# Optimization experiments

Measured on AMD Instinct MI355X. Metric: run time of the kernel, lower is better.

## Reference

```python
import jax, jax.numpy as jnp
import numpy as np

NBITS = 4
QN, QP = -(2 ** (NBITS - 1)), 2 ** (NBITS - 1) - 1  # -8, 7
NUM_HEADS = 12


def round_ste(x):
    # round_pass: straight-through estimator round
    return x + jax.lax.stop_gradient(jnp.round(x) - x)


def act3b(x, alpha, bias=0.0, signed=True):
    qn, qp = (-4.0, 3.0) if signed else (0.0, 7.0)
    return round_ste(jnp.clip((x + bias) / alpha, qn, qp))


def setup_inputs() -> dict:
    key = jax.random.key(0)
    ks = jax.random.split(key, 20)
    B, N, C, H = 32, 512, 768, NUM_HEADS
    hd = C // H
    u = lambda k, s: jax.random.uniform(k, s, jnp.float32, 0.05, 0.15)
    return {
        'x0': jax.random.normal(ks[0], (B, N, C), jnp.float32),
        'qkv_w': 0.02 * jax.random.normal(ks[1], (3 * C, C), jnp.float32),
        'qkv_alpha': u(ks[2], (3 * C,)),
        'qkv_bias': 0.02 * jax.random.normal(ks[3], (3 * C,), jnp.float32),
        'qkv_act_alpha': u(ks[4], (C,)),
        'proj_w': 0.02 * jax.random.normal(ks[5], (C, C), jnp.float32),
        'proj_alpha': u(ks[6], (C,)),
        'proj_bias': 0.02 * jax.random.normal(ks[7], (C,), jnp.float32),
        'proj_act_alpha': u(ks[8], (C,)),
        'normq_w': jax.random.uniform(ks[9], (hd,), jnp.float32, 0.8, 1.2),
        'normq_b': 0.01 * jax.random.normal(ks[10], (hd,), jnp.float32),
        'normk_w': jax.random.uniform(ks[11], (hd,), jnp.float32, 0.8, 1.2),
        'normk_b': 0.01 * jax.random.normal(ks[12], (hd,), jnp.float32),
        'qact_alpha': u(ks[13], (H,)),
        'kact_alpha': u(ks[14], (H,)),
        'vact_alpha': u(ks[15], (H,)),
        'attnact_alpha': u(ks[16], (H,)),
    }


def reference(x0, qkv_w, qkv_alpha, qkv_bias, qkv_act_alpha, proj_w, proj_alpha,
              proj_bias, proj_act_alpha, normq_w, normq_b, normk_w, normk_b,
              qact_alpha, kact_alpha, vact_alpha, attnact_alpha):
    B, N, C = x0.shape
    H = NUM_HEADS
    hd = C // H
    scale = hd ** -0.5

    # input activation quant (ActQ_v2, nbits=4)
    a_in = qkv_act_alpha.mean()
    x0_q = round_ste(jnp.clip(x0 / a_in, QN, QP))
    # kernel-wise 4-bit weight quant for qkv (no dequant here; scales folded later)
    w_q = round_ste(jnp.clip(qkv_w / qkv_alpha[:, None], QN, QP))
    qkv = x0_q @ w_q.T
    # integer-domain bias (truncated toward zero, like .int())
    qkv = qkv + jnp.trunc(qkv_bias / a_in / qkv_alpha)

    qkv = qkv.reshape(B, N, 3, H, hd).transpose(2, 0, 3, 1, 4)  # [3,B,H,N,hd]
    q0, k0, v0 = qkv[0], qkv[1], qkv[2]
    alpha3 = qkv_alpha.reshape(3, H, 1, hd)

    # fused scaled LayerNorm + 3-bit quant for q and k
    def norm_quant(x, ch_scale, nw, nb, act_a):
        xs = x * ch_scale  # [B,H,N,hd]
        centered = xs - xs.mean(-1, keepdims=True)
        std = jnp.std(xs, axis=-1, ddof=1, keepdims=True)
        return act3b(centered / (std + 1e-5), alpha=act_a / nw, bias=nb / nw)

    q2 = norm_quant(q0, alpha3[0], normq_w, normq_b, qact_alpha.mean())
    k2 = norm_quant(k0, alpha3[1], normk_w, normk_b, kact_alpha.mean())
    v2 = act3b(v0, alpha=vact_alpha.mean() / (a_in * alpha3[2]))

    # integer QK^T
    qk = jnp.einsum('bhqd,bhkd->bhqk', q2, k2)

    # base-2 softmax approximation
    div = 128.0
    sm_scale = scale * qact_alpha.mean() * kact_alpha.mean()
    e = jnp.trunc((1.0 / np.log(2)) * sm_scale * qk * div)
    attn_exp = jnp.exp2(jnp.round(e / div))
    attn = act3b(attn_exp / attn_exp.sum(-1, keepdims=True),
                 alpha=attnact_alpha.mean(), signed=False)

    # integer AV
    x1 = jnp.einsum('bhqk,bhkd->bhqd', attn, v2)
    x1 = x1.transpose(0, 2, 1, 3).reshape(B, N, C)
    x1_q = act3b(x1, alpha=proj_act_alpha.mean() / (attnact_alpha.mean() * vact_alpha.mean()))

    pw_q = round_ste(jnp.clip(proj_w / proj_alpha[:, None], QN, QP))
    out = (x1_q @ pw_q.T) * proj_alpha * proj_act_alpha.mean() + proj_bias
    return out
```

## Files before the change

### kernel.cpp

```cpp
#include <hip/hip_runtime.h>
#include <stdint.h>


#define BB 32
#define NN 512
#define CC 768
#define HH 12
#define HD 64
#define M_ROWS (BB * NN)
#define QKV_C (3 * CC)
#define KTA ((size_t)M_ROWS * 64)
#define KTB ((size_t)QKV_C * 64)
#define KTP ((size_t)CC * 64)

typedef int v4i __attribute__((ext_vector_type(4)));
typedef int v16i __attribute__((ext_vector_type(16)));

__device__ __forceinline__ float fadd(float a, float b) { return __fadd_rn(a, b); }
__device__ __forceinline__ float fmul(float a, float b) { return __fmul_rn(a, b); }
__device__ __forceinline__ float fdiv(float a, float b) { return __fdiv_rn(a, b); }
__device__ __forceinline__ float fsub(float a, float b) { return __fsub_rn(a, b); }

__device__ float np_sum_96(const float* a) {
  float r[8];
#pragma unroll
  for (int j = 0; j < 8; j++) r[j] = a[j];
  for (int i = 8; i < 96; i += 8)
#pragma unroll
    for (int j = 0; j < 8; j++) r[j] = fadd(r[j], a[i + j]);
  return fadd(fadd(fadd(r[0], r[1]), fadd(r[2], r[3])),
              fadd(fadd(r[4], r[5]), fadd(r[6], r[7])));
}

__device__ float np_mean_12(const float* a) {
  float r[8];
#pragma unroll
  for (int j = 0; j < 8; j++) r[j] = a[j];
  float res = fadd(fadd(fadd(r[0], r[1]), fadd(r[2], r[3])),
                   fadd(fadd(r[4], r[5]), fadd(r[6], r[7])));
  res = fadd(res, a[8]);
  res = fadd(res, a[9]);
  res = fadd(res, a[10]);
  res = fadd(res, a[11]);
  return fdiv(res, 12.0f);
}

__global__ void prep_kernel(const float* __restrict__ qkv_act_alpha,
                            const float* __restrict__ proj_act_alpha,
                            const float* __restrict__ qact_alpha,
                            const float* __restrict__ kact_alpha,
                            const float* __restrict__ vact_alpha,
                            const float* __restrict__ attnact_alpha,
                            const float* __restrict__ normq_w,
                            const float* __restrict__ normq_b,
                            const float* __restrict__ normk_w,
                            const float* __restrict__ normk_b,
                            const float* __restrict__ qkv_bias,
                            const float* __restrict__ qkv_alpha,
                            float* __restrict__ scal,
                            float* __restrict__ qparams,
                            float* __restrict__ biasq) {
  __shared__ float s_scal[8];
  __shared__ float chunk[16];
  int tid = threadIdx.x;
  if (tid < 8) chunk[tid] = np_sum_96(qkv_act_alpha + 96 * tid);
  else if (tid < 16) chunk[tid] = np_sum_96(proj_act_alpha + 96 * (tid - 8));
  if (tid == 16) s_scal[1] = np_mean_12(qact_alpha);
  if (tid == 17) s_scal[2] = np_mean_12(kact_alpha);
  if (tid == 18) s_scal[3] = np_mean_12(vact_alpha);
  if (tid == 19) s_scal[4] = np_mean_12(attnact_alpha);
  __syncthreads();
  if (tid == 0) {
    float s0 = fadd(fadd(chunk[0], chunk[1]), fadd(chunk[2], chunk[3]));
    float s1 = fadd(fadd(chunk[4], chunk[5]), fadd(chunk[6], chunk[7]));
    s_scal[0] = fdiv(fadd(s0, s1), 768.0f);
    float p0 = fadd(fadd(chunk[8], chunk[9]), fadd(chunk[10], chunk[11]));
    float p1 = fadd(fadd(chunk[12], chunk[13]), fadd(chunk[14], chunk[15]));
    s_scal[5] = fdiv(fadd(p0, p1), 768.0f);
  }
  __syncthreads();
  if (tid < 6) scal[tid] = s_scal[tid];
  if (tid < 64) {
    qparams[tid]       = fdiv(s_scal[1], normq_w[tid]);
    qparams[64 + tid]  = fdiv(normq_b[tid], normq_w[tid]);
    qparams[128 + tid] = fdiv(s_scal[2], normk_w[tid]);
    qparams[192 + tid] = fdiv(normk_b[tid], normk_w[tid]);
  }
  float a_in = s_scal[0];
  for (int c = tid; c < QKV_C; c += blockDim.x)
    biasq[c] = truncf(fdiv(fdiv(qkv_bias[c], a_in), qkv_alpha[c]));
}

__device__ __forceinline__ size_t fragaddr(int row, int b) {
  return (size_t)(row & ~31) * 64 + ((b >> 4) * 512 + (row & 31) * 16 + (b & 15));
}

__global__ void quant_x0_kernel(const float* __restrict__ x0,
                                const float* __restrict__ scal,
                                int8_t* __restrict__ x0q, int total4) {
  int i = blockIdx.x * blockDim.x + threadIdx.x;
  if (i >= total4) return;
  float a_in = scal[0];
  float4 v = ((const float4*)x0)[i];
  char4 o;
  o.x = (int8_t)rintf(fminf(fmaxf(fdiv(v.x, a_in), -8.f), 7.f));
  o.y = (int8_t)rintf(fminf(fmaxf(fdiv(v.y, a_in), -8.f), 7.f));
  o.z = (int8_t)rintf(fminf(fmaxf(fdiv(v.z, a_in), -8.f), 7.f));
  o.w = (int8_t)rintf(fminf(fmaxf(fdiv(v.w, a_in), -8.f), 7.f));
  int seq = i / 192;
  int kp = (i - seq * 192) * 4;
  int b = kp & 63;
  *(char4*)(x0q + (size_t)(kp >> 6) * KTA + fragaddr(seq, b)) = o;
}

__global__ void quant_w_kernel(const float* __restrict__ w,
                               const float* __restrict__ alpha,
                               int8_t* __restrict__ wq, int rows, int total) {
  int i = blockIdx.x * blockDim.x + threadIdx.x;
  if (i >= total) return;
  int row = i / CC;
  int k = i - row * CC;
  float t = fminf(fmaxf(fdiv(w[i], alpha[row]), -8.f), 7.f);
  wq[(size_t)(k >> 6) * ((size_t)rows * 64) + fragaddr(row, k)] =
      (int8_t)rintf(t);
}

__global__ __launch_bounds__(256, 5) void gemm_qkv_kernel(
    const int8_t* __restrict__ Aq, const int8_t* __restrict__ Wq,
    const float* __restrict__ biasq, const float* __restrict__ scal,
    const float* __restrict__ qkv_alpha, const float* __restrict__ qparams,
    int8_t* __restrict__ q2, int8_t* __restrict__ k2,
    int8_t* __restrict__ v2t) {
  __shared__ __align__(16) int8_t packT[4][3072];

  const int L = blockIdx.x;
  const int xcd = L & 7, s = L >> 3;
  const int rb = xcd + 8 * (s / 36);
  const int g = s % 36;
  const int tid = threadIdx.x;
  const int w = tid >> 6, lane = tid & 63;
  const int l31 = lane & 31, hi = lane >> 5;
  const int sec = g / HH, head = g % HH;
  const int col0 = g * 64;
  const int b_idx = rb >> 2, nbase = (rb & 3) * 128;
  const int w32 = w * 32;
  const size_t bh = (size_t)b_idx * HH + head;

  v16i acc0 = (v16i)(0), acc1 = (v16i)(0);

  const int8_t* pa = Aq + (size_t)(rb * 128 + w32) * 64 + hi * 512 + l31 * 16;
  const int8_t* pb = Wq + (size_t)col0 * 64 + hi * 512 + l31 * 16;

  if (sec < 2) {
    v4i Aa = *(const v4i*)(pa);
    v4i Ab = *(const v4i*)(pa + 1024);
    v4i B0a = *(const v4i*)(pb);
    v4i B0b = *(const v4i*)(pb + 1024);
    v4i B1a = *(const v4i*)(pb + 2048);
    v4i B1b = *(const v4i*)(pb + 3072);
#pragma unroll 1
    for (int kt = 0; kt < 11; kt++) {
      const int8_t* npa = pa + (size_t)(kt + 1) * KTA;
      const int8_t* npb = pb + (size_t)(kt + 1) * KTB;
      v4i nAa = *(const v4i*)(npa);
      v4i nAb = *(const v4i*)(npa + 1024);
      v4i nB0a = *(const v4i*)(npb);
      v4i nB0b = *(const v4i*)(npb + 1024);
      v4i nB1a = *(const v4i*)(npb + 2048);
      v4i nB1b = *(const v4i*)(npb + 3072);
      acc0 = __builtin_amdgcn_mfma_i32_32x32x32_i8(B0a, Aa, acc0, 0, 0, 0);
      acc1 = __builtin_amdgcn_mfma_i32_32x32x32_i8(B1a, Aa, acc1, 0, 0, 0);
      acc0 = __builtin_amdgcn_mfma_i32_32x32x32_i8(B0b, Ab, acc0, 0, 0, 0);
      acc1 = __builtin_amdgcn_mfma_i32_32x32x32_i8(B1b, Ab, acc1, 0, 0, 0);
      Aa = nAa; Ab = nAb; B0a = nB0a; B0b = nB0b; B1a = nB1a; B1b = nB1b;
    }
    acc0 = __builtin_amdgcn_mfma_i32_32x32x32_i8(B0a, Aa, acc0, 0, 0, 0);
    acc1 = __builtin_amdgcn_mfma_i32_32x32x32_i8(B1a, Aa, acc1, 0, 0, 0);
    acc0 = __builtin_amdgcn_mfma_i32_32x32x32_i8(B0b, Ab, acc0, 0, 0, 0);
    acc1 = __builtin_amdgcn_mfma_i32_32x32x32_i8(B1b, Ab, acc1, 0, 0, 0);
    float xs[2][16];
#pragma unroll
    for (int i = 0; i < 2; i++)
#pragma unroll
      for (int b = 0; b < 4; b++) {
        int cg = col0 + 32 * i + 8 * b + 4 * hi;
        float4 bqv = *(const float4*)(biasq + cg);
        float4 alv = *(const float4*)(qkv_alpha + cg);
        const float* bqp = (const float*)&bqv;
        const float* alp = (const float*)&alv;
#pragma unroll
        for (int c = 0; c < 4; c++) {
          int av = (i == 0) ? acc0[4 * b + c] : acc1[4 * b + c];
          xs[i][4 * b + c] = fmul(fadd((float)av, bqp[c]), alp[c]);
        }
      }
    float rc[4];
#pragma unroll
    for (int c = 0; c < 4; c++) rc[c] = xs[0][c];
#pragma unroll
    for (int b = 1; b < 4; b++)
#pragma unroll
      for (int c = 0; c < 4; c++) rc[c] = fadd(rc[c], xs[0][4 * b + c]);
#pragma unroll
    for (int b = 0; b < 4; b++)
#pragma unroll
      for (int c = 0; c < 4; c++) rc[c] = fadd(rc[c], xs[1][4 * b + c]);
    float Ls = fadd(fadd(rc[0], rc[1]), fadd(rc[2], rc[3]));
    float Rs = __shfl_xor(Ls, 32, 64);
    float mn = fdiv(fadd(Ls, Rs), 64.0f);
    float vc[4];
#pragma unroll
    for (int c = 0; c < 4; c++) {
      float d = fsub(xs[0][c], mn);
      vc[c] = fmul(d, d);
    }
#pragma unroll
    for (int b = 1; b < 4; b++)
#pragma unroll
      for (int c = 0; c < 4; c++) {
        float d = fsub(xs[0][4 * b + c], mn);
        vc[c] = fadd(vc[c], fmul(d, d));
      }
#pragma unroll
    for (int b = 0; b < 4; b++)
#pragma unroll
      for (int c = 0; c < 4; c++) {
        float d = fsub(xs[1][4 * b + c], mn);
        vc[c] = fadd(vc[c], fmul(d, d));
      }
    float Lv = fadd(fadd(vc[0], vc[1]), fadd(vc[2], vc[3]));
    float Rv = __shfl_xor(Lv, 32, 64);
    float var = fdiv(fadd(Lv, Rv), 63.0f);
    float den = fadd(__fsqrt_rn(var), 1e-5f);
    const float* ap = qparams + (sec == 0 ? 0 : 128);
#pragma unroll
    for (int i = 0; i < 2; i++)
#pragma unroll
      for (int b = 0; b < 4; b++) {
        int cin = 32 * i + 8 * b + 4 * hi;
        float4 a4 = *(const float4*)(ap + cin);
        float4 b4 = *(const float4*)(ap + 64 + cin);
        const float* a4p = (const float*)&a4;
        const float* b4p = (const float*)&b4;
        uint32_t pk = 0;
#pragma unroll
        for (int c = 0; c < 4; c++) {
          float xn = fdiv(fsub(xs[i][4 * b + c], mn), den);
          float t = fdiv(fadd(xn, b4p[c]), a4p[c]);
          t = fminf(fmaxf(t, -4.f), 3.f);
          pk |= ((uint32_t)(uint8_t)(int8_t)rintf(t)) << (8 * c);
        }
        *(uint32_t*)&packT[w][l31 * 80 + cin] = pk;
      }
    asm volatile("s_waitcnt lgkmcnt(0)" ::: "memory");
    int8_t* dst = (sec == 0) ? q2 : k2;
    size_t rowbase = bh * NN + nbase + w32;
#pragma unroll
    for (int c = 0; c < 2; c++) {
      int id = lane + 64 * c;
      int row = id >> 2, off = (id & 3) * 16;
      int4 ov = *(const int4*)&packT[w][row * 80 + off];
      *(int4*)(dst + (rowbase + row) * 64 + off) = ov;
    }
  } else {
    v4i Aa = *(const v4i*)(pa);
    v4i Ab = *(const v4i*)(pa + 1024);
    v4i B0a = *(const v4i*)(pb);
    v4i B0b = *(const v4i*)(pb + 1024);
    v4i B1a = *(const v4i*)(pb + 2048);
    v4i B1b = *(const v4i*)(pb + 3072);
#pragma unroll 1
    for (int kt = 0; kt < 11; kt++) {
      const int8_t* npa = pa + (size_t)(kt + 1) * KTA;
      const int8_t* npb = pb + (size_t)(kt + 1) * KTB;
      v4i nAa = *(const v4i*)(npa);
      v4i nAb = *(const v4i*)(npa + 1024);
      v4i nB0a = *(const v4i*)(npb);
      v4i nB0b = *(const v4i*)(npb + 1024);
      v4i nB1a = *(const v4i*)(npb + 2048);
      v4i nB1b = *(const v4i*)(npb + 3072);
      acc0 = __builtin_amdgcn_mfma_i32_32x32x32_i8(Aa, B0a, acc0, 0, 0, 0);
      acc1 = __builtin_amdgcn_mfma_i32_32x32x32_i8(Aa, B1a, acc1, 0, 0, 0);
      acc0 = __builtin_amdgcn_mfma_i32_32x32x32_i8(Ab, B0b, acc0, 0, 0, 0);
      acc1 = __builtin_amdgcn_mfma_i32_32x32x32_i8(Ab, B1b, acc1, 0, 0, 0);
      Aa = nAa; Ab = nAb; B0a = nB0a; B0b = nB0b; B1a = nB1a; B1b = nB1b;
    }
    acc0 = __builtin_amdgcn_mfma_i32_32x32x32_i8(Aa, B0a, acc0, 0, 0, 0);
    acc1 = __builtin_amdgcn_mfma_i32_32x32x32_i8(Aa, B1a, acc1, 0, 0, 0);
    acc0 = __builtin_amdgcn_mfma_i32_32x32x32_i8(Ab, B0b, acc0, 0, 0, 0);
    acc1 = __builtin_amdgcn_mfma_i32_32x32x32_i8(Ab, B1b, acc1, 0, 0, 0);
    const float a_in = scal[0], vact = scal[3];
#pragma unroll
    for (int sj = 0; sj < 2; sj++) {
      int cg = col0 + 32 * sj + l31;
      float bq = biasq[cg];
      float va = fdiv(vact, fmul(a_in, qkv_alpha[cg]));
      int dloc = 32 * sj + l31;
#pragma unroll
      for (int b = 0; b < 4; b++) {
        uint32_t pk = 0;
#pragma unroll
        for (int c = 0; c < 4; c++) {
          int av = (sj == 0) ? acc0[4 * b + c] : acc1[4 * b + c];
          float vint = fadd((float)av, bq);
          float t = fminf(fmaxf(fdiv(vint, va), -4.f), 3.f);
          pk |= ((uint32_t)(uint8_t)(int8_t)rintf(t)) << (8 * c);
        }
        *(uint32_t*)&packT[w][dloc * 48 + 8 * b + 4 * hi] = pk;
      }
    }
    asm volatile("s_waitcnt lgkmcnt(0)" ::: "memory");
#pragma unroll
    for (int c = 0; c < 2; c++) {
      int id = lane + 64 * c;
      int row = id >> 1, off = (id & 1) * 16;
      int4 ov = *(const int4*)&packT[w][row * 48 + off];
      *(int4*)(v2t + (bh * HD + row) * NN + nbase + w32 + off) = ov;
    }
  }
}

__global__ __launch_bounds__(256) void attn_kernel(
    const int8_t* __restrict__ q2, const int8_t* __restrict__ k2,
    const int8_t* __restrict__ v2t, const float* __restrict__ scal,
    int8_t* __restrict__ x1q) {
  __shared__ __align__(16) int8_t Qs[64][80];
  __shared__ __align__(16) int8_t Ks[64][80];
  __shared__ __align__(16) int8_t Vt[64][80];
  __shared__ __align__(16) int8_t At[64][80];

  const int L = blockIdx.x;
  const int xcd = L & 7, s = L >> 3;
  const int bh = xcd + 8 * (s >> 3);
  const int qt = s & 7;
  const int tid = threadIdx.x;
  const int w = tid >> 6, lane = tid & 63, quad = lane >> 4, c16 = lane & 15;
  const int sr = tid >> 2, scol = (tid & 3) << 4;
  const float attnm = scal[4];
  const float coef =
      fmul(1.4426950408889634f, fmul(fmul(0.125f, scal[1]), scal[2]));
  const float coef128 = fmul(coef, 128.f);
  const size_t base = (size_t)bh * NN * HD;

  *(int4*)&Qs[sr][scol] =
      *(const int4*)(q2 + base + (size_t)(qt * 64 + sr) * HD + scol);
  __syncthreads();
  v4i qf = *(const v4i*)&Qs[16 * w + c16][quad * 16];

  uint32_t mpack[8][4];
  float Srow = 0.f;
  int4 kv = *(const int4*)(k2 + base + (size_t)sr * HD + scol);
#pragma unroll
  for (int kt = 0; kt < 8; kt++) {
    *(int4*)&Ks[sr][scol] = kv;
    __syncthreads();
    if (kt < 7)
      kv = *(const int4*)(k2 + base + (size_t)((kt + 1) * 64 + sr) * HD + scol);
    float psum = 0.f;
#pragma unroll
    for (int f = 0; f < 4; f++) {
      v4i kf = *(const v4i*)&Ks[16 * f + c16][quad * 16];
      v4i d2 = (v4i){0, 0, 0, 0};
      d2 = __builtin_amdgcn_mfma_i32_16x16x64_i8(kf, qf, d2, 0, 0, 0);
      uint32_t pk = 0;
#pragma unroll
      for (int r = 0; r < 4; r++) {
        float e = truncf(fmul(coef128, (float)d2[r]));
        int mi = (int)rintf(fmul(e, 0.0078125f));
        psum = fadd(psum, ldexpf(1.0f, mi));
        pk |= ((uint32_t)(uint8_t)(int8_t)mi) << (8 * r);
      }
      mpack[kt][f] = pk;
    }
    psum = fadd(psum, __shfl_xor(psum, 16, 64));
    psum = fadd(psum, __shfl_xor(psum, 32, 64));
    Srow = fadd(Srow, psum);
    __syncthreads();
  }
  const float u = fdiv(fdiv(1.0f, Srow), attnm);

  v4i xacc[4];
#pragma unroll
  for (int s2 = 0; s2 < 4; s2++) xacc[s2] = (v4i){0, 0, 0, 0};

  int4 vv = *(const int4*)(v2t + ((size_t)bh * HD + sr) * NN + scol);
#pragma unroll
  for (int kt = 0; kt < 8; kt++) {
    *(int4*)&Vt[sr][scol] = vv;
    __syncthreads();
    if (kt < 7)
      vv = *(const int4*)(v2t + ((size_t)bh * HD + sr) * NN + (kt + 1) * 64 +
                          scol);
#pragma unroll
    for (int f = 0; f < 4; f++) {
      uint32_t pk = mpack[kt][f];
      uint32_t wpk = 0;
#pragma unroll
      for (int r = 0; r < 4; r++) {
        int mi = (int)(int8_t)(pk >> (8 * r));
        float t = fminf(ldexpf(u, mi), 7.f);
        wpk |= ((uint32_t)(uint8_t)(int8_t)rintf(t)) << (8 * r);
      }
      *(uint32_t*)&At[16 * w + c16][16 * f + 4 * quad] = wpk;
    }
    asm volatile("s_waitcnt lgkmcnt(0)" ::: "memory");
    v4i af = *(const v4i*)&At[16 * w + c16][quad * 16];
#pragma unroll
    for (int s2 = 0; s2 < 4; s2++) {
      v4i vf = *(const v4i*)&Vt[16 * s2 + c16][quad * 16];
      xacc[s2] = __builtin_amdgcn_mfma_i32_16x16x64_i8(vf, af, xacc[s2], 0, 0, 0);
    }
    __syncthreads();
  }

  const float pa = fdiv(scal[5], fmul(attnm, scal[3]));
#pragma unroll
  for (int s2 = 0; s2 < 4; s2++) {
    uint32_t pack = 0;
#pragma unroll
    for (int r = 0; r < 4; r++) {
      float t = fminf(fmaxf(fdiv((float)xacc[s2][r], pa), -4.f), 3.f);
      pack |= ((uint32_t)(uint8_t)(int8_t)rintf(t)) << (8 * r);
    }
    *(uint32_t*)&Ks[16 * w + c16][16 * s2 + 4 * quad] = pack;
  }
  __syncthreads();
  int4 ov = *(const int4*)&Ks[sr][scol];
  *(int4*)(x1q + ((size_t)bh * NN + qt * 64 + sr) * HD + scol) = ov;
}

__global__ __launch_bounds__(256, 5) void gemm_proj_kernel(
    const int8_t* __restrict__ x1q, const int8_t* __restrict__ Wq,
    const float* __restrict__ proj_alpha, const float* __restrict__ proj_bias,
    const float* __restrict__ scal, float* __restrict__ out) {
  const int L = blockIdx.x;
  const int xcd = L & 7, s = L >> 3;
  const int rb = xcd + 8 * (s / 12);
  const int g = s % 12;
  const int tid = threadIdx.x;
  const int w = tid >> 6, lane = tid & 63;
  const int l31 = lane & 31, hi = lane >> 5;
  const int col0 = g * 64;
  const int b_idx = rb >> 2, nbase = (rb & 3) * 128;
  const int w32 = w * 32;

  v16i acc0 = (v16i)(0), acc1 = (v16i)(0);

  const int8_t* pa =
      x1q + ((size_t)b_idx * HH * NN + nbase + w32 + l31) * 64 + hi * 16;
  const int8_t* pb = Wq + (size_t)col0 * 64 + hi * 512 + l31 * 16;
  const size_t KTX = (size_t)NN * 64;

  v4i Aa = *(const v4i*)(pa);
  v4i Ab = *(const v4i*)(pa + 32);
  v4i B0a = *(const v4i*)(pb);
  v4i B0b = *(const v4i*)(pb + 1024);
  v4i B1a = *(const v4i*)(pb + 2048);
  v4i B1b = *(const v4i*)(pb + 3072);
#pragma unroll 1
  for (int kt = 0; kt < 11; kt++) {
    const int8_t* npa = pa + (size_t)(kt + 1) * KTX;
    const int8_t* npb = pb + (size_t)(kt + 1) * KTP;
    v4i nAa = *(const v4i*)(npa);
    v4i nAb = *(const v4i*)(npa + 32);
    v4i nB0a = *(const v4i*)(npb);
    v4i nB0b = *(const v4i*)(npb + 1024);
    v4i nB1a = *(const v4i*)(npb + 2048);
    v4i nB1b = *(const v4i*)(npb + 3072);
    acc0 = __builtin_amdgcn_mfma_i32_32x32x32_i8(B0a, Aa, acc0, 0, 0, 0);
    acc1 = __builtin_amdgcn_mfma_i32_32x32x32_i8(B1a, Aa, acc1, 0, 0, 0);
    acc0 = __builtin_amdgcn_mfma_i32_32x32x32_i8(B0b, Ab, acc0, 0, 0, 0);
    acc1 = __builtin_amdgcn_mfma_i32_32x32x32_i8(B1b, Ab, acc1, 0, 0, 0);
    Aa = nAa; Ab = nAb; B0a = nB0a; B0b = nB0b; B1a = nB1a; B1b = nB1b;
  }
  acc0 = __builtin_amdgcn_mfma_i32_32x32x32_i8(B0a, Aa, acc0, 0, 0, 0);
  acc1 = __builtin_amdgcn_mfma_i32_32x32x32_i8(B1a, Aa, acc1, 0, 0, 0);
  acc0 = __builtin_amdgcn_mfma_i32_32x32x32_i8(B0b, Ab, acc0, 0, 0, 0);
  acc1 = __builtin_amdgcn_mfma_i32_32x32x32_i8(B1b, Ab, acc1, 0, 0, 0);

  const float pact = scal[5];
  const int m = rb * 128 + w32 + l31;
#pragma unroll
  for (int i = 0; i < 2; i++)
#pragma unroll
    for (int b = 0; b < 4; b++) {
      int colb = col0 + 32 * i + 8 * b + 4 * hi;
      float4 al = *(const float4*)(proj_alpha + colb);
      float4 bi = *(const float4*)(proj_bias + colb);
      const float* alp = (const float*)&al;
      const float* bip = (const float*)&bi;
      float4 o;
      float* op = (float*)&o;
#pragma unroll
      for (int c = 0; c < 4; c++) {
        int av = (i == 0) ? acc0[4 * b + c] : acc1[4 * b + c];
        op[c] = fadd(fmul(fmul((float)av, alp[c]), pact), bip[c]);
      }
      *(float4*)(out + (size_t)m * CC + colb) = o;
    }
}

extern "C" void kernel_launch(void* const* d_in, const int* in_sizes, int n_in,
                              void* d_out, int out_size, void* d_ws,
                              size_t ws_size, hipStream_t stream) {
  const float* x0 = (const float*)d_in[0];
  const float* qkv_w = (const float*)d_in[1];
  const float* qkv_alpha = (const float*)d_in[2];
  const float* qkv_bias = (const float*)d_in[3];
  const float* qkv_act_alpha = (const float*)d_in[4];
  const float* proj_w = (const float*)d_in[5];
  const float* proj_alpha = (const float*)d_in[6];
  const float* proj_bias = (const float*)d_in[7];
  const float* proj_act_alpha = (const float*)d_in[8];
  const float* normq_w = (const float*)d_in[9];
  const float* normq_b = (const float*)d_in[10];
  const float* normk_w = (const float*)d_in[11];
  const float* normk_b = (const float*)d_in[12];
  const float* qact_alpha = (const float*)d_in[13];
  const float* kact_alpha = (const float*)d_in[14];
  const float* vact_alpha = (const float*)d_in[15];
  const float* attnact_alpha = (const float*)d_in[16];

  char* ws = (char*)d_ws;
  size_t off = 0;
  auto alloc = [&](size_t bytes) -> char* {
    char* p = ws + off;
    off += (bytes + 255) & ~(size_t)255;
    return p;
  };
  float* scal = (float*)alloc(64 * 4);
  float* qparams = (float*)alloc(256 * 4);
  float* biasq = (float*)alloc(QKV_C * 4);
  int8_t* x0q = (int8_t*)alloc((size_t)M_ROWS * CC);
  int8_t* wq = (int8_t*)alloc((size_t)QKV_C * CC);
  int8_t* pwq = (int8_t*)alloc((size_t)CC * CC);
  int8_t* q2 = (int8_t*)alloc((size_t)BB * HH * NN * HD);
  int8_t* k2 = (int8_t*)alloc((size_t)BB * HH * NN * HD);
  int8_t* v2t = (int8_t*)alloc((size_t)BB * HH * NN * HD);
  int8_t* x1q = (int8_t*)alloc((size_t)M_ROWS * CC);

  prep_kernel<<<1, 256, 0, stream>>>(qkv_act_alpha, proj_act_alpha, qact_alpha,
                                     kact_alpha, vact_alpha, attnact_alpha,
                                     normq_w, normq_b, normk_w, normk_b,
                                     qkv_bias, qkv_alpha, scal, qparams, biasq);

  int total4 = M_ROWS * CC / 4;
  quant_x0_kernel<<<(total4 + 255) / 256, 256, 0, stream>>>(x0, scal, x0q,
                                                            total4);
  quant_w_kernel<<<(QKV_C * CC + 255) / 256, 256, 0, stream>>>(
      qkv_w, qkv_alpha, wq, QKV_C, QKV_C * CC);
  quant_w_kernel<<<(CC * CC + 255) / 256, 256, 0, stream>>>(
      proj_w, proj_alpha, pwq, CC, CC * CC);

  gemm_qkv_kernel<<<36 * (M_ROWS / 128), 256, 0, stream>>>(
      x0q, wq, biasq, scal, qkv_alpha, qparams, q2, k2, v2t);

  attn_kernel<<<(NN / 64) * (BB * HH), 256, 0, stream>>>(q2, k2, v2t, scal,
                                                         x1q);

  gemm_proj_kernel<<<12 * (M_ROWS / 128), 256, 0, stream>>>(
      x1q, pwq, proj_alpha, proj_bias, scal, (float*)d_out);
}
```

Before: 304.2 us.

## Store V in MFMA fragment layout and load K/V fragments directly to registers

```diff
diff --git a/kernel.cpp b/kernel.cpp
--- a/kernel.cpp
+++ b/kernel.cpp
@@ -130,7 +130,7 @@
     const float* __restrict__ biasq, const float* __restrict__ scal,
     const float* __restrict__ qkv_alpha, const float* __restrict__ qparams,
     int8_t* __restrict__ q2, int8_t* __restrict__ k2,
-    int8_t* __restrict__ v2t) {
+    int8_t* __restrict__ v2f) {
   __shared__ __align__(16) int8_t packT[4][3072];
 
   const int L = blockIdx.x;
@@ -315,18 +315,18 @@
       int id = lane + 64 * c;
       int row = id >> 1, off = (id & 1) * 16;
       int4 ov = *(const int4*)&packT[w][row * 48 + off];
-      *(int4*)(v2t + (bh * HD + row) * NN + nbase + w32 + off) = ov;
-    }
-  }
-}
-
-__global__ __launch_bounds__(256) void attn_kernel(
+      int n0 = nbase + w32 + off;
+      *(int4*)(v2f + (size_t)bh * 32768 + ((n0 >> 6) * 4096) +
+               ((row >> 4) * 1024) + ((row & 15) * 64) +
+               (((n0 >> 4) & 3) * 16)) = ov;
+    }
+  }
+}
+
+__global__ __launch_bounds__(256, 4) void attn_kernel(
     const int8_t* __restrict__ q2, const int8_t* __restrict__ k2,
-    const int8_t* __restrict__ v2t, const float* __restrict__ scal,
+    const int8_t* __restrict__ v2f, const float* __restrict__ scal,
     int8_t* __restrict__ x1q) {
-  __shared__ __align__(16) int8_t Qs[64][80];
-  __shared__ __align__(16) int8_t Ks[64][80];
-  __shared__ __align__(16) int8_t Vt[64][80];
   __shared__ __align__(16) int8_t At[64][80];
 
   const int L = blockIdx.x;
@@ -342,24 +342,25 @@
   const float coef128 = fmul(coef, 128.f);
   const size_t base = (size_t)bh * NN * HD;
 
-  *(int4*)&Qs[sr][scol] =
-      *(const int4*)(q2 + base + (size_t)(qt * 64 + sr) * HD + scol);
-  __syncthreads();
-  v4i qf = *(const v4i*)&Qs[16 * w + c16][quad * 16];
+  const int8_t* kptr = k2 + base + (size_t)c16 * 64 + quad * 16;
+  const int8_t* vptr = v2f + base + (size_t)c16 * 64 + quad * 16;
+  v4i qf = *(const v4i*)(q2 + base + (size_t)(qt * 64 + 16 * w + c16) * 64 +
+                         quad * 16);
 
   uint32_t mpack[8][4];
   float Srow = 0.f;
-  int4 kv = *(const int4*)(k2 + base + (size_t)sr * HD + scol);
+  v4i kfr[4];
+#pragma unroll
+  for (int f = 0; f < 4; f++)
+    kfr[f] = *(const v4i*)(kptr + f * 1024);
 #pragma unroll
   for (int kt = 0; kt < 8; kt++) {
-    *(int4*)&Ks[sr][scol] = kv;
-    __syncthreads();
-    if (kt < 7)
-      kv = *(const int4*)(k2 + base + (size_t)((kt + 1) * 64 + sr) * HD + scol);
     float psum = 0.f;
 #pragma unroll
     for (int f = 0; f < 4; f++) {
-      v4i kf = *(const v4i*)&Ks[16 * f + c16][quad * 16];
+      v4i kf = kfr[f];
+      if (kt < 7)
+        kfr[f] = *(const v4i*)(kptr + (kt + 1) * 4096 + f * 1024);
       v4i d2 = (v4i){0, 0, 0, 0};
       d2 = __builtin_amdgcn_mfma_i32_16x16x64_i8(kf, qf, d2, 0, 0, 0);
       uint32_t pk = 0;
@@ -375,22 +376,19 @@
     psum = fadd(psum, __shfl_xor(psum, 16, 64));
     psum = fadd(psum, __shfl_xor(psum, 32, 64));
     Srow = fadd(Srow, psum);
-    __syncthreads();
   }
   const float u = fdiv(fdiv(1.0f, Srow), attnm);
 
   v4i xacc[4];
 #pragma unroll
   for (int s2 = 0; s2 < 4; s2++) xacc[s2] = (v4i){0, 0, 0, 0};
-
-  int4 vv = *(const int4*)(v2t + ((size_t)bh * HD + sr) * NN + scol);
+  v4i vfr[4];
+#pragma unroll
+  for (int s2 = 0; s2 < 4; s2++)
+    vfr[s2] = *(const v4i*)(vptr + s2 * 1024);
+
 #pragma unroll
   for (int kt = 0; kt < 8; kt++) {
-    *(int4*)&Vt[sr][scol] = vv;
-    __syncthreads();
-    if (kt < 7)
-      vv = *(const int4*)(v2t + ((size_t)bh * HD + sr) * NN + (kt + 1) * 64 +
-                          scol);
 #pragma unroll
     for (int f = 0; f < 4; f++) {
       uint32_t pk = mpack[kt][f];
@@ -407,10 +405,11 @@
     v4i af = *(const v4i*)&At[16 * w + c16][quad * 16];
 #pragma unroll
     for (int s2 = 0; s2 < 4; s2++) {
-      v4i vf = *(const v4i*)&Vt[16 * s2 + c16][quad * 16];
+      v4i vf = vfr[s2];
+      if (kt < 7)
+        vfr[s2] = *(const v4i*)(vptr + (kt + 1) * 4096 + s2 * 1024);
       xacc[s2] = __builtin_amdgcn_mfma_i32_16x16x64_i8(vf, af, xacc[s2], 0, 0, 0);
     }
-    __syncthreads();
   }
 
   const float pa = fdiv(scal[5], fmul(attnm, scal[3]));
@@ -422,10 +421,10 @@
       float t = fminf(fmaxf(fdiv((float)xacc[s2][r], pa), -4.f), 3.f);
       pack |= ((uint32_t)(uint8_t)(int8_t)rintf(t)) << (8 * r);
     }
-    *(uint32_t*)&Ks[16 * w + c16][16 * s2 + 4 * quad] = pack;
+    *(uint32_t*)&At[16 * w + c16][16 * s2 + 4 * quad] = pack;
   }
   __syncthreads();
-  int4 ov = *(const int4*)&Ks[sr][scol];
+  int4 ov = *(const int4*)&At[sr][scol];
   *(int4*)(x1q + ((size_t)bh * NN + qt * 64 + sr) * HD + scol) = ov;
 }
 
@@ -536,7 +535,7 @@
   int8_t* pwq = (int8_t*)alloc((size_t)CC * CC);
   int8_t* q2 = (int8_t*)alloc((size_t)BB * HH * NN * HD);
   int8_t* k2 = (int8_t*)alloc((size_t)BB * HH * NN * HD);
-  int8_t* v2t = (int8_t*)alloc((size_t)BB * HH * NN * HD);
+  int8_t* v2f = (int8_t*)alloc((size_t)BB * HH * NN * HD);
   int8_t* x1q = (int8_t*)alloc((size_t)M_ROWS * CC);
 
   prep_kernel<<<1, 256, 0, stream>>>(qkv_act_alpha, proj_act_alpha, qact_alpha,
@@ -553,9 +552,9 @@
       proj_w, proj_alpha, pwq, CC, CC * CC);
 
   gemm_qkv_kernel<<<36 * (M_ROWS / 128), 256, 0, stream>>>(
-      x0q, wq, biasq, scal, qkv_alpha, qparams, q2, k2, v2t);
-
-  attn_kernel<<<(NN / 64) * (BB * HH), 256, 0, stream>>>(q2, k2, v2t, scal,
+      x0q, wq, biasq, scal, qkv_alpha, qparams, q2, k2, v2f);
+
+  attn_kernel<<<(NN / 64) * (BB * HH), 256, 0, stream>>>(q2, k2, v2f, scal,
                                                          x1q);
 
   gemm_proj_kernel<<<12 * (M_ROWS / 128), 256, 0, stream>>>(
```

After: 382.3 us. 25.7% more time.
